# Performance work log

Measured on AMD Instinct MI355X. Metric: run time of the kernel, lower is better.

The kernel has to match this reference:

```python
import jax, jax.numpy as jnp
import numpy as np

N_NODES = 100000
N_EDGES = 1600000
IN_CH = 48
OUT_CH = 48
BN_EPS = 1e-5


def setup_inputs() -> dict:
    key = jax.random.key(0)
    k1, k2, k3, k4 = jax.random.split(key, 4)
    x = jax.random.normal(k1, (N_NODES, IN_CH), dtype=jnp.float32)
    edge_index = jax.random.randint(k2, (2, N_EDGES), 0, N_NODES, dtype=jnp.int32)
    # GCNConv linear weight (glorot) and bias
    W = jax.random.normal(k3, (IN_CH, OUT_CH), dtype=jnp.float32) * (1.0 / np.sqrt(IN_CH))
    b = jnp.zeros((OUT_CH,), dtype=jnp.float32)
    # BatchNorm affine params
    gamma = jnp.ones((OUT_CH,), dtype=jnp.float32)
    beta = jnp.zeros((OUT_CH,), dtype=jnp.float32)
    return {"x": x, "edge_index": edge_index, "W": W, "b": b, "gamma": gamma, "beta": beta}


def reference(x, edge_index, W, b, gamma, beta):
    N = x.shape[0]
    # --- GCNConv: add self loops ---
    loops = jnp.arange(N, dtype=edge_index.dtype)
    src = jnp.concatenate([edge_index[0], loops])
    dst = jnp.concatenate([edge_index[1], loops])
    # symmetric normalization: deg counted at destination (incl. self loops)
    deg = jax.ops.segment_sum(jnp.ones_like(dst, dtype=x.dtype), dst, num_segments=N)
    dinv = jax.lax.rsqrt(deg)  # deg >= 1 due to self loops
    norm = dinv[src] * dinv[dst]  # [E+N]
    # linear transform first (small GEMM), then gather-scale-scatter
    h = x @ W  # [N, OUT_CH]
    msg = h[src] * norm[:, None]  # [E+N, OUT_CH]
    agg = jax.ops.segment_sum(msg, dst, num_segments=N) + b  # [N, OUT_CH]
    # --- BatchNorm1d (training mode: batch statistics, biased variance) ---
    mean = jnp.mean(agg, axis=0)
    var = jnp.mean(jnp.square(agg - mean), axis=0)
    y = (agg - mean) * jax.lax.rsqrt(var + BN_EPS) * gamma + beta
    # --- ReLU ---
    return jax.nn.relu(y)
```

## Files before the change

kernel.cpp:

```cpp
#include <hip/hip_runtime.h>
#include <hip/hip_bf16.h>

#define IN_CH 48
#define OUT_CH 48
#define BN_EPS 1e-5f
#define CHUNK 4096
#define EPT   16
#define NPB   256
#define NHB   512

__device__ __forceinline__ float bf2f(ushort u) {
    union { unsigned int i; float f; } v;
    v.i = ((unsigned int)u) << 16;
    return v.f;
}
__device__ __forceinline__ ushort f2bf(float f) {
    __hip_bfloat16 h = __float2bfloat16(f);
    return *(ushort*)&h;
}

__global__ __launch_bounds__(512) void k_zero(int* __restrict__ bhist) {
    bhist[threadIdx.x] = 0;
}

__global__ __launch_bounds__(256) void k_binhist(const int* __restrict__ dst,
                                                 int* __restrict__ bhist, int E) {
    __shared__ int h[512];
    int t = threadIdx.x;
    h[t] = 0; h[t + 256] = 0;
    __syncthreads();
    const int stride = NHB * 256;
    int e = blockIdx.x * 256 + t;
    for (; e + 3 * stride < E; e += 4 * stride) {
        int d0 = dst[e];
        int d1 = dst[e + stride];
        int d2 = dst[e + 2 * stride];
        int d3 = dst[e + 3 * stride];
        atomicAdd(&h[d0 >> 8], 1);
        atomicAdd(&h[d1 >> 8], 1);
        atomicAdd(&h[d2 >> 8], 1);
        atomicAdd(&h[d3 >> 8], 1);
    }
    for (; e < E; e += stride) atomicAdd(&h[dst[e] >> 8], 1);
    __syncthreads();
    if (h[t]) atomicAdd(&bhist[t], h[t]);
    if (h[t + 256]) atomicAdd(&bhist[t + 256], h[t + 256]);
}

__global__ __launch_bounds__(256) void k_scanb(const int* __restrict__ bhist,
                                               int* __restrict__ bstart,
                                               int* __restrict__ bcur, int nb,
                                               float* __restrict__ stats) {
    __shared__ int sc[256];
    int t = threadIdx.x;
    if (t < 128) stats[t] = 0.0f;
    int i0 = 2 * t, i1 = 2 * t + 1;
    int a0 = bhist[i0];
    int a1 = bhist[i1];
    int ps = a0 + a1;
    sc[t] = ps;
    __syncthreads();
    for (int off = 1; off < 256; off <<= 1) {
        int v = (t >= off) ? sc[t - off] : 0;
        __syncthreads();
        sc[t] += v;
        __syncthreads();
    }
    int excl = sc[t] - ps;
    bstart[i0] = excl;
    bstart[i1] = excl + a0;
    if (i0 < nb) bcur[i0] = excl;
    if (i1 < nb) bcur[i1] = excl + a0;
    if (t == 255) bstart[512] = sc[255];
}

union alignas(16) SMem {
    struct {
        int hist[512];
        int hbase[513];
        int sc[256];
        int gb[512];
        unsigned int stage[CHUNK];
        short stagebk[CHUNK];
    } bin;
    float Wl[IN_CH * OUT_CH];
};

__global__ __launch_bounds__(256) void k_binmm(const int* __restrict__ src,
                                               const int* __restrict__ dst,
                                               int* __restrict__ bcur,
                                               unsigned int* __restrict__ binned,
                                               int E, int nchunks,
                                               const float* __restrict__ x,
                                               const float* __restrict__ W,
                                               ushort* __restrict__ g, int N) {
    __shared__ SMem sm;
    int t = threadIdx.x;

    if (blockIdx.x < nchunks) {
        int e0 = blockIdx.x * CHUNK;
        int n = min(CHUNK, E - e0);

        sm.bin.hist[t] = 0; sm.bin.hist[t + 256] = 0;
        __syncthreads();

        unsigned int w[EPT];
        short bb[EPT];
#pragma unroll
        for (int k = 0; k < EPT; ++k) {
            int i = t + k * 256;
            if (i < n) {
                int e = e0 + i;
                int s = src[e], d = dst[e];
                int b = d >> 8;
                w[k] = (unsigned int)s | ((unsigned int)(d & 255) << 17);
                bb[k] = (short)b;
                atomicAdd(&sm.bin.hist[b], 1);
            } else bb[k] = -1;
        }
        __syncthreads();
        int a0 = sm.bin.hist[2 * t], a1 = sm.bin.hist[2 * t + 1];
        int ps = a0 + a1;
        sm.bin.sc[t] = ps;
        __syncthreads();
        for (int off = 1; off < 256; off <<= 1) {
            int v = (t >= off) ? sm.bin.sc[t - off] : 0;
            __syncthreads();
            sm.bin.sc[t] += v;
            __syncthreads();
        }
        int excl = sm.bin.sc[t] - ps;
        sm.bin.hbase[2 * t] = excl;
        sm.bin.hbase[2 * t + 1] = excl + a0;
        if (t == 255) sm.bin.hbase[512] = sm.bin.sc[255];
        __syncthreads();
        sm.bin.hist[2 * t] = excl;
        sm.bin.hist[2 * t + 1] = excl + a0;
        __syncthreads();
#pragma unroll
        for (int k = 0; k < EPT; ++k) {
            if (bb[k] >= 0) {
                int pos = atomicAdd(&sm.bin.hist[bb[k]], 1);
                sm.bin.stage[pos] = w[k];
                sm.bin.stagebk[pos] = bb[k];
            }
        }
        __syncthreads();
        for (int b = t; b < 512; b += 256) {
            int cnt = sm.bin.hbase[b + 1] - sm.bin.hbase[b];
            if (cnt > 0) sm.bin.gb[b] = atomicAdd(&bcur[b], cnt) - sm.bin.hbase[b];
        }
        __syncthreads();
        for (int j = t; j < n; j += 256) {
            int bk = sm.bin.stagebk[j];
            binned[sm.bin.gb[bk] + j] = sm.bin.stage[j];
        }
    } else {
        for (int idx = t; idx < IN_CH * OUT_CH / 4; idx += 256)
            ((float4*)sm.Wl)[idx] = ((const float4*)W)[idx];
        __syncthreads();

        int i = (blockIdx.x - nchunks) * 256 + t;
        if (i >= N) return;

        float xr[IN_CH];
        const float4* xp = (const float4*)(x + (size_t)i * IN_CH);
#pragma unroll
        for (int k = 0; k < IN_CH / 4; ++k) {
            float4 v = xp[k];
            xr[4 * k] = v.x; xr[4 * k + 1] = v.y; xr[4 * k + 2] = v.z; xr[4 * k + 3] = v.w;
        }

        ushort row[OUT_CH];
#pragma unroll
        for (int c4 = 0; c4 < OUT_CH / 4; ++c4) {
            float4 acc = make_float4(0.f, 0.f, 0.f, 0.f);
#pragma unroll
            for (int k = 0; k < IN_CH; ++k) {
                float4 wv = ((const float4*)sm.Wl)[k * (OUT_CH / 4) + c4];
                acc.x += xr[k] * wv.x; acc.y += xr[k] * wv.y;
                acc.z += xr[k] * wv.z; acc.w += xr[k] * wv.w;
            }
            row[4 * c4 + 0] = f2bf(acc.x);
            row[4 * c4 + 1] = f2bf(acc.y);
            row[4 * c4 + 2] = f2bf(acc.z);
            row[4 * c4 + 3] = f2bf(acc.w);
        }
        uint4* gp = (uint4*)(g + (size_t)i * OUT_CH);
#pragma unroll
        for (int j = 0; j < 6; ++j) gp[j] = ((uint4*)row)[j];
    }
}

__global__ __launch_bounds__(512) void k_fine(const unsigned int* __restrict__ binned,
                                              const int* __restrict__ bstart,
                                              int* __restrict__ counts,
                                              int* __restrict__ rowstart,
                                              int* __restrict__ sorted_src,
                                              ushort* __restrict__ g, int N) {
    __shared__ int cnt[256];
    __shared__ int sc[256];
    __shared__ int cur[256];
    __shared__ float sdinv[256];
    int b = blockIdx.x, t = threadIdx.x;
    int node0 = b << 8;
    int nn = min(NPB, N - node0);
    if (t < 256) cnt[t] = 0;
    __syncthreads();
    int e0 = bstart[b], e1 = bstart[b + 1];
    for (int e = e0 + t; e < e1; e += 512)
        atomicAdd(&cnt[binned[e] >> 17], 1);
    __syncthreads();
    if (t < 256) sc[t] = cnt[t];
    __syncthreads();
    for (int off = 1; off < 256; off <<= 1) {
        int v = 0;
        if (t < 256 && t >= off) v = sc[t - off];
        __syncthreads();
        if (t < 256) sc[t] += v;
        __syncthreads();
    }
    if (t < 256) {
        int excl = sc[t] - cnt[t];
        cur[t] = e0 + excl;
        sdinv[t] = rsqrtf((float)cnt[t] + 1.0f);
        if (t < nn) {
            counts[node0 + t] = cnt[t];
            rowstart[node0 + t] = e0 + excl;
        }
    }
    __syncthreads();
    for (int e = e0 + t; e < e1; e += 512) {
        unsigned int w = binned[e];
        int dl = (int)(w >> 17);
        int pos = atomicAdd(&cur[dl], 1);
        sorted_src[pos] = (int)(w & 0x1ffff);
    }
    unsigned int* gw = (unsigned int*)(g + (size_t)node0 * OUT_CH);
    int words = nn * (OUT_CH / 2);
    for (int i = t; i < words; i += 512) {
        int r = i / (OUT_CH / 2);
        float d = sdinv[r];
        unsigned int u = gw[i];
        float lo = bf2f((ushort)(u & 0xffff)) * d;
        float hi = bf2f((ushort)(u >> 16)) * d;
        gw[i] = (unsigned int)f2bf(lo) | ((unsigned int)f2bf(hi) << 16);
    }
}

__global__ __launch_bounds__(256) void k_gather(const int* __restrict__ sorted_src,
                                                const int* __restrict__ rowstart,
                                                const int* __restrict__ counts,
                                                const ushort* __restrict__ g,
                                                float* __restrict__ out, int N) {
    int t = blockIdx.x * blockDim.x + threadIdx.x;
    if (t >= N * 12) return;
    int node = t / 12;
    int sub = t - node * 12;
    const uint2* gp = (const uint2*)g;
    int cnt = counts[node];
    int e = rowstart[node];
    int end = e + cnt;

    uint2 sv = gp[(size_t)node * 12 + sub];
    float a0 = bf2f((ushort)(sv.x & 0xffff));
    float a1 = bf2f((ushort)(sv.x >> 16));
    float a2 = bf2f((ushort)(sv.y & 0xffff));
    float a3 = bf2f((ushort)(sv.y >> 16));

    for (; e + 4 <= end; e += 4) {
        int s0 = sorted_src[e];
        int s1 = sorted_src[e + 1];
        int s2 = sorted_src[e + 2];
        int s3 = sorted_src[e + 3];
        uint2 v0 = gp[(size_t)s0 * 12 + sub];
        uint2 v1 = gp[(size_t)s1 * 12 + sub];
        uint2 v2 = gp[(size_t)s2 * 12 + sub];
        uint2 v3 = gp[(size_t)s3 * 12 + sub];
        a0 += bf2f((ushort)(v0.x & 0xffff)) + bf2f((ushort)(v1.x & 0xffff))
            + bf2f((ushort)(v2.x & 0xffff)) + bf2f((ushort)(v3.x & 0xffff));
        a1 += bf2f((ushort)(v0.x >> 16)) + bf2f((ushort)(v1.x >> 16))
            + bf2f((ushort)(v2.x >> 16)) + bf2f((ushort)(v3.x >> 16));
        a2 += bf2f((ushort)(v0.y & 0xffff)) + bf2f((ushort)(v1.y & 0xffff))
            + bf2f((ushort)(v2.y & 0xffff)) + bf2f((ushort)(v3.y & 0xffff));
        a3 += bf2f((ushort)(v0.y >> 16)) + bf2f((ushort)(v1.y >> 16))
            + bf2f((ushort)(v2.y >> 16)) + bf2f((ushort)(v3.y >> 16));
    }
    for (; e < end; ++e) {
        int s = sorted_src[e];
        uint2 v = gp[(size_t)s * 12 + sub];
        a0 += bf2f((ushort)(v.x & 0xffff));
        a1 += bf2f((ushort)(v.x >> 16));
        a2 += bf2f((ushort)(v.y & 0xffff));
        a3 += bf2f((ushort)(v.y >> 16));
    }
    float di = rsqrtf((float)cnt + 1.0f);
    float4 r;
    r.x = a0 * di; r.y = a1 * di; r.z = a2 * di; r.w = a3 * di;
    ((float4*)out)[(size_t)node * 12 + sub] = r;
}

__global__ __launch_bounds__(768) void k_stats(const float* __restrict__ v,
                                               float* __restrict__ stats, int N) {
    __shared__ float ls[16][OUT_CH];
    __shared__ float ls2[16][OUT_CH];
    int c = threadIdx.x;
    int ty = threadIdx.y;
    float s = 0.f, s2 = 0.f;
    for (int r = blockIdx.x * 16 + ty; r < N; r += gridDim.x * 16) {
        float u = v[(size_t)r * OUT_CH + c];
        s += u;
        s2 += u * u;
    }
    ls[ty][c] = s;
    ls2[ty][c] = s2;
    __syncthreads();
    for (int h = 8; h > 0; h >>= 1) {
        if (ty < h) {
            ls[ty][c] += ls[ty + h][c];
            ls2[ty][c] += ls2[ty + h][c];
        }
        __syncthreads();
    }
    if (ty == 0) {
        atomicAdd(&stats[c], ls[0][c]);
        atomicAdd(&stats[OUT_CH + c], ls2[0][c]);
    }
}

__global__ void k_final(float* __restrict__ out, const float* __restrict__ stats,
                        const float* __restrict__ gamma,
                        const float* __restrict__ beta, int N) {
    int t = blockIdx.x * blockDim.x + threadIdx.x;
    int total = N * OUT_CH;
    if (t >= total) return;
    int c = t % OUT_CH;
    float invN = 1.0f / (float)N;
    float m = stats[c] * invN;
    float var = stats[OUT_CH + c] * invN - m * m;
    float y = (out[t] - m) * rsqrtf(var + BN_EPS) * gamma[c] + beta[c];
    out[t] = fmaxf(y, 0.0f);
}

extern "C" void kernel_launch(void* const* d_in, const int* in_sizes, int n_in,
                              void* d_out, int out_size, void* d_ws, size_t ws_size,
                              hipStream_t stream) {
    const float* x     = (const float*)d_in[0];
    const int*   ei    = (const int*)d_in[1];
    const float* W     = (const float*)d_in[2];
    const float* gamma = (const float*)d_in[4];
    const float* beta  = (const float*)d_in[5];
    float*       out   = (float*)d_out;

    int N = in_sizes[0] / IN_CH;
    int E = in_sizes[1] / 2;
    const int* src = ei;
    const int* dst = ei + E;

    int nb = (N + NPB - 1) / NPB;

    char* wsb = (char*)d_ws;
    float*        stats      = (float*)wsb;
    int*          bstart     = (int*)(wsb + 512);
    int*          bcur       = (int*)(wsb + 4096);
    int*          bhist      = (int*)(wsb + 8192);
    size_t A = 139264;
    int*          counts     = (int*)(wsb + A);
    int*          rowstart   = (int*)(wsb + A + (size_t)4 * N);
    unsigned int* binned     = (unsigned int*)(wsb + A + (size_t)8 * N);
    int*          sorted_src = (int*)(wsb + A + (size_t)8 * N + (size_t)4 * E);
    ushort*       g          = (ushort*)(wsb + A + (size_t)8 * N + (size_t)8 * E);

    int b = 256;
    int nchunks = (E + CHUNK - 1) / CHUNK;
    int ngemm = (N + b - 1) / b;

    k_zero<<<1, 512, 0, stream>>>(bhist);
    k_binhist<<<NHB, b, 0, stream>>>(dst, bhist, E);
    k_scanb<<<1, b, 0, stream>>>(bhist, bstart, bcur, nb, stats);
    k_binmm<<<nchunks + ngemm, b, 0, stream>>>(src, dst, bcur, binned, E, nchunks,
                                               x, W, g, N);
    k_fine<<<nb, 512, 0, stream>>>(binned, bstart, counts, rowstart, sorted_src, g, N);
    int gthreads = N * 12;
    k_gather<<<(gthreads + b - 1) / b, b, 0, stream>>>(sorted_src, rowstart, counts, g, out, N);
    dim3 sblk(OUT_CH, 16);
    k_stats<<<256, sblk, 0, stream>>>(out, stats, N);
    int totalT = N * OUT_CH;
    k_final<<<(totalT + b - 1) / b, b, 0, stream>>>(out, stats, gamma, beta, N);
}
```

Baseline: 130.1 us.

## Fuse BN statistics into gather kernel and widen gather loads to 16 bytes

The gather kernel now has each thread handle 8 channels with uint4 loads, using 6 threads per node instead of 12. It accumulates per-block channel sums and sums of squares in shared memory via LDS atomics and writes them to per-block partials. A small reduction kernel then produces the final stats, replacing the separate pass that re-read the whole output. This removes one full read of the output and the global float atomics, at the cost of LDS atomic contention and fewer threads in the latency-bound gather.

```diff
diff --git a/kernel.cpp b/kernel.cpp
--- a/kernel.cpp
+++ b/kernel.cpp
@@ -49,11 +49,9 @@
 
 __global__ __launch_bounds__(256) void k_scanb(const int* __restrict__ bhist,
                                                int* __restrict__ bstart,
-                                               int* __restrict__ bcur, int nb,
-                                               float* __restrict__ stats) {
+                                               int* __restrict__ bcur, int nb) {
     __shared__ int sc[256];
     int t = threadIdx.x;
-    if (t < 128) stats[t] = 0.0f;
     int i0 = 2 * t, i1 = 2 * t + 1;
     int a0 = bhist[i0];
     int a1 = bhist[i1];
@@ -252,80 +250,101 @@
                                                 const int* __restrict__ rowstart,
                                                 const int* __restrict__ counts,
                                                 const ushort* __restrict__ g,
-                                                float* __restrict__ out, int N) {
-    int t = blockIdx.x * blockDim.x + threadIdx.x;
-    if (t >= N * 12) return;
-    int node = t / 12;
-    int sub = t - node * 12;
-    const uint2* gp = (const uint2*)g;
-    int cnt = counts[node];
-    int e = rowstart[node];
-    int end = e + cnt;
-
-    uint2 sv = gp[(size_t)node * 12 + sub];
-    float a0 = bf2f((ushort)(sv.x & 0xffff));
-    float a1 = bf2f((ushort)(sv.x >> 16));
-    float a2 = bf2f((ushort)(sv.y & 0xffff));
-    float a3 = bf2f((ushort)(sv.y >> 16));
-
-    for (; e + 4 <= end; e += 4) {
-        int s0 = sorted_src[e];
-        int s1 = sorted_src[e + 1];
-        int s2 = sorted_src[e + 2];
-        int s3 = sorted_src[e + 3];
-        uint2 v0 = gp[(size_t)s0 * 12 + sub];
-        uint2 v1 = gp[(size_t)s1 * 12 + sub];
-        uint2 v2 = gp[(size_t)s2 * 12 + sub];
-        uint2 v3 = gp[(size_t)s3 * 12 + sub];
-        a0 += bf2f((ushort)(v0.x & 0xffff)) + bf2f((ushort)(v1.x & 0xffff))
-            + bf2f((ushort)(v2.x & 0xffff)) + bf2f((ushort)(v3.x & 0xffff));
-        a1 += bf2f((ushort)(v0.x >> 16)) + bf2f((ushort)(v1.x >> 16))
-            + bf2f((ushort)(v2.x >> 16)) + bf2f((ushort)(v3.x >> 16));
-        a2 += bf2f((ushort)(v0.y & 0xffff)) + bf2f((ushort)(v1.y & 0xffff))
-            + bf2f((ushort)(v2.y & 0xffff)) + bf2f((ushort)(v3.y & 0xffff));
-        a3 += bf2f((ushort)(v0.y >> 16)) + bf2f((ushort)(v1.y >> 16))
-            + bf2f((ushort)(v2.y >> 16)) + bf2f((ushort)(v3.y >> 16));
-    }
-    for (; e < end; ++e) {
-        int s = sorted_src[e];
-        uint2 v = gp[(size_t)s * 12 + sub];
-        a0 += bf2f((ushort)(v.x & 0xffff));
-        a1 += bf2f((ushort)(v.x >> 16));
-        a2 += bf2f((ushort)(v.y & 0xffff));
-        a3 += bf2f((ushort)(v.y >> 16));
-    }
-    float di = rsqrtf((float)cnt + 1.0f);
-    float4 r;
-    r.x = a0 * di; r.y = a1 * di; r.z = a2 * di; r.w = a3 * di;
-    ((float4*)out)[(size_t)node * 12 + sub] = r;
-}
-
-__global__ __launch_bounds__(768) void k_stats(const float* __restrict__ v,
-                                               float* __restrict__ stats, int N) {
-    __shared__ float ls[16][OUT_CH];
-    __shared__ float ls2[16][OUT_CH];
-    int c = threadIdx.x;
-    int ty = threadIdx.y;
-    float s = 0.f, s2 = 0.f;
-    for (int r = blockIdx.x * 16 + ty; r < N; r += gridDim.x * 16) {
-        float u = v[(size_t)r * OUT_CH + c];
-        s += u;
-        s2 += u * u;
-    }
-    ls[ty][c] = s;
-    ls2[ty][c] = s2;
-    __syncthreads();
-    for (int h = 8; h > 0; h >>= 1) {
-        if (ty < h) {
-            ls[ty][c] += ls[ty + h][c];
-            ls2[ty][c] += ls2[ty + h][c];
-        }
-        __syncthreads();
-    }
-    if (ty == 0) {
-        atomicAdd(&stats[c], ls[0][c]);
-        atomicAdd(&stats[OUT_CH + c], ls2[0][c]);
-    }
+                                                float* __restrict__ out,
+                                                float* __restrict__ spart, int N) {
+    __shared__ float ssum[OUT_CH];
+    __shared__ float ssq[OUT_CH];
+    int lt = threadIdx.x;
+    if (lt < OUT_CH) { ssum[lt] = 0.0f; ssq[lt] = 0.0f; }
+    __syncthreads();
+
+    int t = blockIdx.x * 256 + lt;
+    bool valid = (t < N * 6);
+    if (valid) {
+        int node = t / 6;
+        int sub = t - node * 6;
+        const uint4* gp = (const uint4*)g;
+        int cnt = counts[node];
+        int e = rowstart[node];
+        int end = e + cnt;
+
+        uint4 sv = gp[(size_t)node * 6 + sub];
+        float a0 = bf2f((ushort)(sv.x & 0xffff)), a1 = bf2f((ushort)(sv.x >> 16));
+        float a2 = bf2f((ushort)(sv.y & 0xffff)), a3 = bf2f((ushort)(sv.y >> 16));
+        float a4 = bf2f((ushort)(sv.z & 0xffff)), a5 = bf2f((ushort)(sv.z >> 16));
+        float a6 = bf2f((ushort)(sv.w & 0xffff)), a7 = bf2f((ushort)(sv.w >> 16));
+
+        for (; e + 4 <= end; e += 4) {
+            int s0 = sorted_src[e];
+            int s1 = sorted_src[e + 1];
+            int s2 = sorted_src[e + 2];
+            int s3 = sorted_src[e + 3];
+            uint4 v0 = gp[(size_t)s0 * 6 + sub];
+            uint4 v1 = gp[(size_t)s1 * 6 + sub];
+            uint4 v2 = gp[(size_t)s2 * 6 + sub];
+            uint4 v3 = gp[(size_t)s3 * 6 + sub];
+            a0 += bf2f((ushort)(v0.x & 0xffff)) + bf2f((ushort)(v1.x & 0xffff))
+                + bf2f((ushort)(v2.x & 0xffff)) + bf2f((ushort)(v3.x & 0xffff));
+            a1 += bf2f((ushort)(v0.x >> 16)) + bf2f((ushort)(v1.x >> 16))
+                + bf2f((ushort)(v2.x >> 16)) + bf2f((ushort)(v3.x >> 16));
+            a2 += bf2f((ushort)(v0.y & 0xffff)) + bf2f((ushort)(v1.y & 0xffff))
+                + bf2f((ushort)(v2.y & 0xffff)) + bf2f((ushort)(v3.y & 0xffff));
+            a3 += bf2f((ushort)(v0.y >> 16)) + bf2f((ushort)(v1.y >> 16))
+                + bf2f((ushort)(v2.y >> 16)) + bf2f((ushort)(v3.y >> 16));
+            a4 += bf2f((ushort)(v0.z & 0xffff)) + bf2f((ushort)(v1.z & 0xffff))
+                + bf2f((ushort)(v2.z & 0xffff)) + bf2f((ushort)(v3.z & 0xffff));
+            a5 += bf2f((ushort)(v0.z >> 16)) + bf2f((ushort)(v1.z >> 16))
+                + bf2f((ushort)(v2.z >> 16)) + bf2f((ushort)(v3.z >> 16));
+            a6 += bf2f((ushort)(v0.w & 0xffff)) + bf2f((ushort)(v1.w & 0xffff))
+                + bf2f((ushort)(v2.w & 0xffff)) + bf2f((ushort)(v3.w & 0xffff));
+            a7 += bf2f((ushort)(v0.w >> 16)) + bf2f((ushort)(v1.w >> 16))
+                + bf2f((ushort)(v2.w >> 16)) + bf2f((ushort)(v3.w >> 16));
+        }
+        for (; e < end; ++e) {
+            int s = sorted_src[e];
+            uint4 v = gp[(size_t)s * 6 + sub];
+            a0 += bf2f((ushort)(v.x & 0xffff)); a1 += bf2f((ushort)(v.x >> 16));
+            a2 += bf2f((ushort)(v.y & 0xffff)); a3 += bf2f((ushort)(v.y >> 16));
+            a4 += bf2f((ushort)(v.z & 0xffff)); a5 += bf2f((ushort)(v.z >> 16));
+            a6 += bf2f((ushort)(v.w & 0xffff)); a7 += bf2f((ushort)(v.w >> 16));
+        }
+        float di = rsqrtf((float)cnt + 1.0f);
+        a0 *= di; a1 *= di; a2 *= di; a3 *= di;
+        a4 *= di; a5 *= di; a6 *= di; a7 *= di;
+        float4* op = (float4*)(out + (size_t)node * OUT_CH + sub * 8);
+        op[0] = make_float4(a0, a1, a2, a3);
+        op[1] = make_float4(a4, a5, a6, a7);
+        int c = 8 * sub;
+        atomicAdd(&ssum[c + 0], a0); atomicAdd(&ssum[c + 1], a1);
+        atomicAdd(&ssum[c + 2], a2); atomicAdd(&ssum[c + 3], a3);
+        atomicAdd(&ssum[c + 4], a4); atomicAdd(&ssum[c + 5], a5);
+        atomicAdd(&ssum[c + 6], a6); atomicAdd(&ssum[c + 7], a7);
+        atomicAdd(&ssq[c + 0], a0 * a0); atomicAdd(&ssq[c + 1], a1 * a1);
+        atomicAdd(&ssq[c + 2], a2 * a2); atomicAdd(&ssq[c + 3], a3 * a3);
+        atomicAdd(&ssq[c + 4], a4 * a4); atomicAdd(&ssq[c + 5], a5 * a5);
+        atomicAdd(&ssq[c + 6], a6 * a6); atomicAdd(&ssq[c + 7], a7 * a7);
+    }
+    __syncthreads();
+    if (lt < OUT_CH) {
+        spart[(size_t)blockIdx.x * 96 + lt] = ssum[lt];
+        spart[(size_t)blockIdx.x * 96 + OUT_CH + lt] = ssq[lt];
+    }
+}
+
+__global__ __launch_bounds__(256) void k_redstats(const float* __restrict__ spart,
+                                                  float* __restrict__ stats, int nblk) {
+    __shared__ float l[256];
+    int c = blockIdx.x;
+    int t = threadIdx.x;
+    float s = 0.f;
+    for (int b = t; b < nblk; b += 256) s += spart[(size_t)b * 96 + c];
+    l[t] = s;
+    __syncthreads();
+    for (int h = 128; h > 0; h >>= 1) {
+        if (t < h) l[t] += l[t + h];
+        __syncthreads();
+    }
+    if (t == 0) stats[c] = l[0];
 }
 
 __global__ void k_final(float* __restrict__ out, const float* __restrict__ stats,
@@ -370,6 +389,7 @@
     unsigned int* binned     = (unsigned int*)(wsb + A + (size_t)8 * N);
     int*          sorted_src = (int*)(wsb + A + (size_t)8 * N + (size_t)4 * E);
     ushort*       g          = (ushort*)(wsb + A + (size_t)8 * N + (size_t)8 * E);
+    float*        spart      = (float*)(wsb + A + (size_t)8 * N + (size_t)8 * E + (size_t)96 * N);
 
     int b = 256;
     int nchunks = (E + CHUNK - 1) / CHUNK;
@@ -377,14 +397,14 @@
 
     k_zero<<<1, 512, 0, stream>>>(bhist);
     k_binhist<<<NHB, b, 0, stream>>>(dst, bhist, E);
-    k_scanb<<<1, b, 0, stream>>>(bhist, bstart, bcur, nb, stats);
+    k_scanb<<<1, b, 0, stream>>>(bhist, bstart, bcur, nb);
     k_binmm<<<nchunks + ngemm, b, 0, stream>>>(src, dst, bcur, binned, E, nchunks,
                                                x, W, g, N);
     k_fine<<<nb, 512, 0, stream>>>(binned, bstart, counts, rowstart, sorted_src, g, N);
-    int gthreads = N * 12;
-    k_gather<<<(gthreads + b - 1) / b, b, 0, stream>>>(sorted_src, rowstart, counts, g, out, N);
-    dim3 sblk(OUT_CH, 16);
-    k_stats<<<256, sblk, 0, stream>>>(out, stats, N);
+    int gthreads = N * 6;
+    int gblocks = (gthreads + b - 1) / b;
+    k_gather<<<gblocks, b, 0, stream>>>(sorted_src, rowstart, counts, g, out, spart, N);
+    k_redstats<<<2 * OUT_CH, b, 0, stream>>>(spart, stats, gblocks);
     int totalT = N * OUT_CH;
     k_final<<<(totalT + b - 1) / b, b, 0, stream>>>(out, stats, gamma, beta, N);
 }
```

Measured after the change: 162.6 us. 1.25x slower.
